# Kernel tuning notes

Hardware: AMD Instinct MI355X
Metric: run time of the kernel (lower is better)

Reference implementation:

```python
import jax, jax.numpy as jnp
import numpy as np
from jax.ops import segment_sum

N_NODES = 100000
N_EDGES = 1600000
N_LABEL = 200000
IN_C, HID_C, OUT_C = 128, 128, 64


def setup_inputs() -> dict:
    key = jax.random.key(0)
    ks = jax.random.split(key, 6)
    x = jax.random.normal(ks[0], (N_NODES, IN_C), dtype=jnp.float32)
    edge_index = jax.random.randint(ks[1], (2, N_EDGES), 0, N_NODES, dtype=jnp.int64)
    edge_label_index = jax.random.randint(ks[2], (2, N_LABEL), 0, N_NODES, dtype=jnp.int64)
    W1 = jax.random.normal(ks[3], (IN_C, HID_C), dtype=jnp.float32) / np.sqrt(IN_C)
    b1 = jnp.zeros((HID_C,), dtype=jnp.float32)
    W2 = jax.random.normal(ks[4], (HID_C, OUT_C), dtype=jnp.float32) / np.sqrt(HID_C)
    b2 = jnp.zeros((OUT_C,), dtype=jnp.float32)
    return {"x": x, "edge_index": edge_index, "edge_label_index": edge_label_index,
            "W1": W1, "b1": b1, "W2": W2, "b2": b2}


def gcn_conv(x, W, b, src, dst, num_nodes):
    # PyG GCNConv: linear transform, add self-loops, symmetric normalization, sum-aggregate, bias.
    h = x @ W                                            # [N, C_out]
    loop = jnp.arange(num_nodes, dtype=src.dtype)
    s = jnp.concatenate([src, loop])                     # [E + N]
    d = jnp.concatenate([dst, loop])
    deg = segment_sum(jnp.ones_like(d, dtype=h.dtype), d, num_segments=num_nodes)
    dinv = jnp.where(deg > 0, jax.lax.rsqrt(deg), 0.0)   # deg^-1/2
    norm = dinv[s] * dinv[d]                             # [E + N]
    msg = h[s] * norm[:, None]                           # gather + scale
    out = segment_sum(msg, d, num_segments=num_nodes)    # scatter-add aggregate
    return out + b


def reference(x, edge_index, edge_label_index, W1, b1, W2, b2):
    src, dst = edge_index[0], edge_index[1]
    n = x.shape[0]
    h = jax.nn.relu(gcn_conv(x, W1, b1, src, dst, n))
    z = gcn_conv(h, W2, b2, src, dst, n)                 # encode
    # decode: dot product over candidate edges
    return jnp.sum(z[edge_label_index[0]] * z[edge_label_index[1]], axis=-1)
```

## Files before the change

kernel.cpp:

```cpp
#include <hip/hip_runtime.h>

typedef __attribute__((ext_vector_type(8))) short bfrag8;
typedef __attribute__((ext_vector_type(4))) float facc4;

__device__ __forceinline__ unsigned int f2bf(float f) {
    unsigned int u = __float_as_uint(f);
    return (u + 0x7FFFu + ((u >> 16) & 1u)) >> 16;
}
__device__ __forceinline__ float bf_lo(unsigned int w) { return __uint_as_float(w << 16); }
__device__ __forceinline__ float bf_hi(unsigned int w) { return __uint_as_float(w & 0xffff0000u); }


__global__ void k_count(const int* __restrict__ dst, int* __restrict__ cnt,
                        unsigned int* __restrict__ pack, int e) {
    int i = blockIdx.x * blockDim.x + threadIdx.x;
    if (i < e) {
        int d = dst[i];
        int r = atomicAdd(&cnt[d], 1);
        pack[i] = ((unsigned int)d << 14) | (unsigned int)r;
    }
}


__global__ void k_cvt(const float* __restrict__ x, const float* __restrict__ W1,
                      const float* __restrict__ W2, unsigned short* __restrict__ x16,
                      unsigned short* __restrict__ w1t, unsigned short* __restrict__ w2t,
                      int nx8) {
    int t = blockIdx.x * blockDim.x + threadIdx.x;
    if (t < nx8) {
        const float4* xp = reinterpret_cast<const float4*>(x) + (long)t * 2;
        float4 a = xp[0], b = xp[1];
        uint4 o;
        o.x = f2bf(a.x) | (f2bf(a.y) << 16);
        o.y = f2bf(a.z) | (f2bf(a.w) << 16);
        o.z = f2bf(b.x) | (f2bf(b.y) << 16);
        o.w = f2bf(b.z) | (f2bf(b.w) << 16);
        reinterpret_cast<uint4*>(x16)[t] = o;
    } else {
        int u = t - nx8;
        if (u < 128 * 128) {
            int k = u >> 7, nn = u & 127;
            w1t[nn * 128 + k] = (unsigned short)f2bf(W1[u]);
        } else if ((u -= 128 * 128) < 128 * 64) {
            int k = u >> 6, nn = u & 63;
            w2t[nn * 128 + k] = (unsigned short)f2bf(W2[u]);
        }
    }
}

#define SCP 1024

__global__ void k_scan_a(const int* __restrict__ cnt, int* __restrict__ part, int n) {
    int p = blockIdx.x * blockDim.x + threadIdx.x;
    if (p >= SCP) return;
    int chunk = (n + SCP - 1) / SCP;
    int b = p * chunk, e = min(b + chunk, n), s = 0;
    for (int i = b; i < e; ++i) s += cnt[i];
    part[p] = s;
}

__global__ void k_scan_b(int* __restrict__ part) {
    __shared__ int sm[SCP];
    int t = threadIdx.x;
    sm[t] = part[t];
    __syncthreads();
    for (int off = 1; off < SCP; off <<= 1) {
        int v = (t >= off) ? sm[t - off] : 0;
        __syncthreads();
        sm[t] += v;
        __syncthreads();
    }
    part[t] = t ? sm[t - 1] : 0;
}

__global__ void k_scan_c(const int* __restrict__ cnt, const int* __restrict__ part,
                         int* __restrict__ rowptr, float* __restrict__ dinv, int n) {
    int p = blockIdx.x * blockDim.x + threadIdx.x;
    if (p >= SCP) return;
    int chunk = (n + SCP - 1) / SCP;
    int b = p * chunk, e = min(b + chunk, n);
    int run = part[p];
    for (int i = b; i < e; ++i) {
        rowptr[i] = run;
        dinv[i] = rsqrtf((float)(cnt[i] + 1));
        run += cnt[i];
    }
    if (p == SCP - 1) rowptr[n] = run;
}


#define FILL_G 192

__device__ __forceinline__ void fill_role(const int* __restrict__ src,
                                          const unsigned int* __restrict__ pack,
                                          const int* __restrict__ rowptr,
                                          int* __restrict__ csr_src,
                                          int e, float scale, int r, int g) {
    int chunk = (e + FILL_G - 1) / FILL_G;
    int beg = g * chunk, end = min(beg + chunk, e);
    for (int i = beg + threadIdx.x; i < end; i += blockDim.x) {
        unsigned int p = pack[i];
        int d = (int)(p >> 14);
        if ((int)((float)d * scale) == r) {
            int pos = rowptr[d] + (int)(p & 0x3FFFu);
            csr_src[pos] = src[i];
        }
    }
}


__global__ __launch_bounds__(256) void k_fuse(
        const int* __restrict__ src, const unsigned int* __restrict__ pack,
        const int* __restrict__ rowptr, int* __restrict__ csr_src, int e, float scale,
        const unsigned short* __restrict__ X16, const unsigned short* __restrict__ W1T,
        const float* __restrict__ dinv, unsigned short* __restrict__ H16, int n) {
    __shared__ unsigned short sA[128 * 64];
    __shared__ unsigned short sB[128 * 64];

    int t8 = blockIdx.x >> 3, l8 = blockIdx.x & 7;
    int m = t8 % 3, q = t8 / 3;

    if (m < 2) {
        int g = q * 2 + m;
        if (g < FILL_G)
            fill_role(src, pack, rowptr, csr_src, e, scale, l8, g);
        return;
    }

    int bid = q * 8 + l8;
    int row0 = bid * 128;
    if (row0 >= n) return;

    int tid = threadIdx.x;
    int lane = tid & 63;
    int wv = tid >> 6;

    facc4 acc[2][8];
#pragma unroll
    for (int i = 0; i < 2; ++i)
#pragma unroll
        for (int j = 0; j < 8; ++j) acc[i][j] = (facc4)0.f;

    for (int s = 0; s < 2; ++s) {
        if (s) __syncthreads();
#pragma unroll
        for (int it = 0; it < 4; ++it) {
            int chunk = it * 4 + wv;
            int L = chunk * 64 + lane;
            int row = L >> 3, gp = L & 7;
            int gsrc = gp ^ (row & 7);
            int grow = min(row0 + row, n - 1);
            const unsigned short* srcp = X16 + (long)grow * 128 + s * 64 + gsrc * 8;
            unsigned short* dstp = sA + chunk * 512;
            __builtin_amdgcn_global_load_lds(
                (const __attribute__((address_space(1))) void*)srcp,
                (__attribute__((address_space(3))) void*)dstp, 16, 0, 0);
        }
#pragma unroll
        for (int it = 0; it < 4; ++it) {
            int chunk = it * 4 + wv;
            int L = chunk * 64 + lane;
            int row = L >> 3, gp = L & 7;
            int gsrc = gp ^ (row & 7);
            const unsigned short* srcp = W1T + (long)row * 128 + s * 64 + gsrc * 8;
            unsigned short* dstp = sB + chunk * 512;
            __builtin_amdgcn_global_load_lds(
                (const __attribute__((address_space(1))) void*)srcp,
                (__attribute__((address_space(3))) void*)dstp, 16, 0, 0);
        }
        __syncthreads();

        bfrag8 af[2][2];
#pragma unroll
        for (int mt = 0; mt < 2; ++mt)
#pragma unroll
            for (int ks = 0; ks < 2; ++ks) {
                int r = wv * 32 + mt * 16 + (lane & 15);
                int g = ks * 4 + (lane >> 4);
                af[mt][ks] = *reinterpret_cast<const bfrag8*>(&sA[r * 64 + (g ^ (r & 7)) * 8]);
            }
#pragma unroll
        for (int nt = 0; nt < 8; ++nt) {
            int nr = nt * 16 + (lane & 15);
            bfrag8 b0 = *reinterpret_cast<const bfrag8*>(&sB[nr * 64 + (((lane >> 4)) ^ (nr & 7)) * 8]);
            bfrag8 b1 = *reinterpret_cast<const bfrag8*>(&sB[nr * 64 + ((4 + (lane >> 4)) ^ (nr & 7)) * 8]);
            acc[0][nt] = __builtin_amdgcn_mfma_f32_16x16x32_bf16(af[0][0], b0, acc[0][nt], 0, 0, 0);
            acc[1][nt] = __builtin_amdgcn_mfma_f32_16x16x32_bf16(af[1][0], b0, acc[1][nt], 0, 0, 0);
            acc[0][nt] = __builtin_amdgcn_mfma_f32_16x16x32_bf16(af[0][1], b1, acc[0][nt], 0, 0, 0);
            acc[1][nt] = __builtin_amdgcn_mfma_f32_16x16x32_bf16(af[1][1], b1, acc[1][nt], 0, 0, 0);
        }
    }

#pragma unroll
    for (int mt = 0; mt < 2; ++mt)
#pragma unroll
        for (int reg = 0; reg < 4; ++reg) {
            int r = row0 + wv * 32 + mt * 16 + (lane >> 4) * 4 + reg;
            if (r < n) {
                float dv = dinv[r];
#pragma unroll
                for (int nt = 0; nt < 8; ++nt)
                    H16[(long)r * 128 + nt * 16 + (lane & 15)] =
                        (unsigned short)f2bf(acc[mt][nt][reg] * dv);
            }
        }
}


__global__ __launch_bounds__(256) void k_gemmM64(const unsigned short* __restrict__ H16,
                                                 const unsigned short* __restrict__ W2T,
                                                 const float* __restrict__ dinv,
                                                 unsigned short* __restrict__ Z16, int n) {
    __shared__ unsigned short sA[128 * 64];
    __shared__ unsigned short sB[64 * 64];

    int row0 = blockIdx.x * 128;
    int tid = threadIdx.x;
    int lane = tid & 63;
    int wv = tid >> 6;

    facc4 acc[2][4];
#pragma unroll
    for (int i = 0; i < 2; ++i)
#pragma unroll
        for (int j = 0; j < 4; ++j) acc[i][j] = (facc4)0.f;

    for (int s = 0; s < 2; ++s) {
        if (s) __syncthreads();
#pragma unroll
        for (int it = 0; it < 4; ++it) {
            int chunk = it * 4 + wv;
            int L = chunk * 64 + lane;
            int row = L >> 3, gp = L & 7;
            int gsrc = gp ^ (row & 7);
            int grow = min(row0 + row, n - 1);
            const unsigned short* srcp = H16 + (long)grow * 128 + s * 64 + gsrc * 8;
            unsigned short* dstp = sA + chunk * 512;
            __builtin_amdgcn_global_load_lds(
                (const __attribute__((address_space(1))) void*)srcp,
                (__attribute__((address_space(3))) void*)dstp, 16, 0, 0);
        }
#pragma unroll
        for (int it = 0; it < 2; ++it) {
            int chunk = it * 4 + wv;
            int L = chunk * 64 + lane;
            int row = L >> 3, gp = L & 7;
            int gsrc = gp ^ (row & 7);
            const unsigned short* srcp = W2T + (long)row * 128 + s * 64 + gsrc * 8;
            unsigned short* dstp = sB + chunk * 512;
            __builtin_amdgcn_global_load_lds(
                (const __attribute__((address_space(1))) void*)srcp,
                (__attribute__((address_space(3))) void*)dstp, 16, 0, 0);
        }
        __syncthreads();

        bfrag8 af[2][2];
#pragma unroll
        for (int mt = 0; mt < 2; ++mt)
#pragma unroll
            for (int ks = 0; ks < 2; ++ks) {
                int r = wv * 32 + mt * 16 + (lane & 15);
                int g = ks * 4 + (lane >> 4);
                af[mt][ks] = *reinterpret_cast<const bfrag8*>(&sA[r * 64 + (g ^ (r & 7)) * 8]);
            }
#pragma unroll
        for (int nt = 0; nt < 4; ++nt) {
            int nr = nt * 16 + (lane & 15);
            bfrag8 b0 = *reinterpret_cast<const bfrag8*>(&sB[nr * 64 + (((lane >> 4)) ^ (nr & 7)) * 8]);
            bfrag8 b1 = *reinterpret_cast<const bfrag8*>(&sB[nr * 64 + ((4 + (lane >> 4)) ^ (nr & 7)) * 8]);
            acc[0][nt] = __builtin_amdgcn_mfma_f32_16x16x32_bf16(af[0][0], b0, acc[0][nt], 0, 0, 0);
            acc[1][nt] = __builtin_amdgcn_mfma_f32_16x16x32_bf16(af[1][0], b0, acc[1][nt], 0, 0, 0);
            acc[0][nt] = __builtin_amdgcn_mfma_f32_16x16x32_bf16(af[0][1], b1, acc[0][nt], 0, 0, 0);
            acc[1][nt] = __builtin_amdgcn_mfma_f32_16x16x32_bf16(af[1][1], b1, acc[1][nt], 0, 0, 0);
        }
    }

#pragma unroll
    for (int mt = 0; mt < 2; ++mt)
#pragma unroll
        for (int reg = 0; reg < 4; ++reg) {
            int r = row0 + wv * 32 + mt * 16 + (lane >> 4) * 4 + reg;
            if (r < n) {
                float dv = dinv[r];
#pragma unroll
                for (int nt = 0; nt < 4; ++nt)
                    Z16[(long)r * 64 + nt * 16 + (lane & 15)] =
                        (unsigned short)f2bf(acc[mt][nt][reg] * dv);
            }
        }
}


template<int C, bool RELU, bool OB>
__global__ void k_gather16(const int* __restrict__ rowptr, const int* __restrict__ csr_src,
                           const float* __restrict__ dinv, const unsigned short* __restrict__ h16,
                           const float* __restrict__ bias, void* __restrict__ outv, int n) {
    const int TPN = C / 8;
    const int RS = C / 8;
    int t = blockIdx.x * blockDim.x + threadIdx.x;
    int node = t / TPN;
    if (node >= n) return;
    int cg = t % TPN;

    const uint4* h4 = reinterpret_cast<const uint4*>(h16);
    float acc[8];
    {
        uint4 u = h4[(long)node * RS + cg];
        acc[0] = bf_lo(u.x); acc[1] = bf_hi(u.x);
        acc[2] = bf_lo(u.y); acc[3] = bf_hi(u.y);
        acc[4] = bf_lo(u.z); acc[5] = bf_hi(u.z);
        acc[6] = bf_lo(u.w); acc[7] = bf_hi(u.w);
    }

    int beg = rowptr[node], end = rowptr[node + 1];
    int e = beg;
    for (; e + 8 <= end; e += 8) {
        int s[8];
#pragma unroll
        for (int q = 0; q < 8; ++q) s[q] = csr_src[e + q];
        uint4 u[8];
#pragma unroll
        for (int q = 0; q < 8; ++q) u[q] = h4[(long)s[q] * RS + cg];
#pragma unroll
        for (int q = 0; q < 8; ++q) {
            acc[0] += bf_lo(u[q].x); acc[1] += bf_hi(u[q].x);
            acc[2] += bf_lo(u[q].y); acc[3] += bf_hi(u[q].y);
            acc[4] += bf_lo(u[q].z); acc[5] += bf_hi(u[q].z);
            acc[6] += bf_lo(u[q].w); acc[7] += bf_hi(u[q].w);
        }
    }
    for (; e < end; ++e) {
        uint4 u = h4[(long)csr_src[e] * RS + cg];
        acc[0] += bf_lo(u.x); acc[1] += bf_hi(u.x);
        acc[2] += bf_lo(u.y); acc[3] += bf_hi(u.y);
        acc[4] += bf_lo(u.z); acc[5] += bf_hi(u.z);
        acc[6] += bf_lo(u.w); acc[7] += bf_hi(u.w);
    }

    float dd = dinv[node];
    int c0 = cg * 8;
    float4 ba = *reinterpret_cast<const float4*>(bias + c0);
    float4 bb = *reinterpret_cast<const float4*>(bias + c0 + 4);
    float o[8];
    o[0] = fmaf(acc[0], dd, ba.x); o[1] = fmaf(acc[1], dd, ba.y);
    o[2] = fmaf(acc[2], dd, ba.z); o[3] = fmaf(acc[3], dd, ba.w);
    o[4] = fmaf(acc[4], dd, bb.x); o[5] = fmaf(acc[5], dd, bb.y);
    o[6] = fmaf(acc[6], dd, bb.z); o[7] = fmaf(acc[7], dd, bb.w);
    if (RELU) {
#pragma unroll
        for (int i = 0; i < 8; ++i) o[i] = fmaxf(o[i], 0.f);
    }
    if (OB) {
        uint4 w;
        w.x = f2bf(o[0]) | (f2bf(o[1]) << 16);
        w.y = f2bf(o[2]) | (f2bf(o[3]) << 16);
        w.z = f2bf(o[4]) | (f2bf(o[5]) << 16);
        w.w = f2bf(o[6]) | (f2bf(o[7]) << 16);
        *reinterpret_cast<uint4*>((unsigned short*)outv + (long)node * C + c0) = w;
    } else {
        float* of = (float*)outv + (long)node * C + c0;
        *reinterpret_cast<float4*>(of) = make_float4(o[0], o[1], o[2], o[3]);
        *reinterpret_cast<float4*>(of + 4) = make_float4(o[4], o[5], o[6], o[7]);
    }
}


__global__ void k_decode(const int* __restrict__ ia, const int* __restrict__ ib,
                         const float* __restrict__ z, float* __restrict__ out, int m) {
    int t = blockIdx.x * blockDim.x + threadIdx.x;
    int k = t / 16;
    if (k >= m) return;
    int c = (t & 15) * 4;
    int a = ia[k], b = ib[k];
    float4 va = *reinterpret_cast<const float4*>(z + (long)a * 64 + c);
    float4 vb = *reinterpret_cast<const float4*>(z + (long)b * 64 + c);
    float dot = va.x * vb.x + va.y * vb.y + va.z * vb.z + va.w * vb.w;
    dot += __shfl_xor(dot, 8);
    dot += __shfl_xor(dot, 4);
    dot += __shfl_xor(dot, 2);
    dot += __shfl_xor(dot, 1);
    if ((t & 15) == 0) out[k] = dot;
}


extern "C" void kernel_launch(void* const* d_in, const int* in_sizes, int n_in,
                              void* d_out, int out_size, void* d_ws, size_t ws_size,
                              hipStream_t stream) {
    const float* x  = (const float*)d_in[0];
    const int*   ei = (const int*)d_in[1];
    const int*   el = (const int*)d_in[2];
    const float* W1 = (const float*)d_in[3];
    const float* b1 = (const float*)d_in[4];
    const float* W2 = (const float*)d_in[5];
    const float* b2 = (const float*)d_in[6];
    float* out = (float*)d_out;

    const int N = in_sizes[0] / 128;
    const int E = in_sizes[1] / 2;
    const int L = out_size;

    const int* src = ei;
    const int* dst = ei + E;
    const int* la  = el;
    const int* lb  = el + L;

    char* wsb = (char*)d_ws;

    unsigned short* ht16 = (unsigned short*)wsb;
    unsigned short* zt16 = (unsigned short*)wsb;
    float*          zout = (float*)(wsb + (size_t)N * 128);

    unsigned int*   pack = (unsigned int*)(wsb + (size_t)N * 512);
    unsigned short* h16  = (unsigned short*)(wsb + (size_t)N * 512);
    unsigned short* x16  = (unsigned short*)(wsb + (size_t)N * 512 + (size_t)N * 256);

    int*   csr_src = (int*)(wsb + (size_t)N * 1024);
    int*   cnt     = csr_src + E;
    int*   rowptr  = cnt + N;
    float* dinv    = (float*)(rowptr + N + 1);
    int*   part    = (int*)(dinv + N);
    unsigned short* w1t = (unsigned short*)(part + SCP);
    unsigned short* w2t = w1t + 128 * 128;

    auto cdiv = [](long a, long b) { return (int)((a + b - 1) / b); };

    int nx8 = N * 16;
    k_cvt<<<cdiv((long)nx8 + 128 * 128 + 128 * 64, 256), 256, 0, stream>>>(
        x, W1, W2, x16, w1t, w2t, nx8);

    hipMemsetAsync(cnt, 0, (size_t)N * sizeof(int), stream);
    k_count <<<cdiv(E, 256), 256, 0, stream>>>(dst, cnt, pack, E);
    k_scan_a<<<SCP / 256, 256, 0, stream>>>(cnt, part, N);
    k_scan_b<<<1, SCP, 0, stream>>>(part);
    k_scan_c<<<SCP / 256, 256, 0, stream>>>(cnt, part, rowptr, dinv, N);

    k_fuse<<<294 * 8, 256, 0, stream>>>(src, pack, rowptr, csr_src, E, 8.0f / (float)N,
                                        x16, w1t, dinv, ht16, N);

    k_gather16<128, true, true><<<cdiv((long)N * 16, 256), 256, 0, stream>>>(
        rowptr, csr_src, dinv, ht16, b1, h16, N);

    k_gemmM64<<<cdiv(N, 128), 256, 0, stream>>>(h16, w2t, dinv, zt16, N);
    k_gather16<64, false, false><<<cdiv((long)N * 8, 256), 256, 0, stream>>>(
        rowptr, csr_src, dinv, zt16, b2, zout, N);

    k_decode<<<cdiv((long)L * 16, 256), 256, 0, stream>>>(la, lb, zout, out, L);
}
```

Measured before the change: 328.5 us.

## Fuse degree count into prep kernel, use atomic cursors, store z in bf16

The separate count kernel is folded into the conversion kernel as extra blocks. Those blocks bucket destination nodes into eight range partitions for atomic locality, and no longer write a packed rank array. The CSR fill now gets slots through atomic cursors initialised by the scan instead of precomputed ranks. The second-layer output is stored as bf16, and decode reads bf16 rows, which halves gather traffic at the cost of precision. Atomic-based fill makes the order within each CSR row nondeterministic and adds atomics in the fill pass.

```diff
diff --git a/kernel.cpp b/kernel.cpp
--- a/kernel.cpp
+++ b/kernel.cpp
@@ -11,30 +11,33 @@
 __device__ __forceinline__ float bf_hi(unsigned int w) { return __uint_as_float(w & 0xffff0000u); }
 
 
-__global__ void k_count(const int* __restrict__ dst, int* __restrict__ cnt,
-                        unsigned int* __restrict__ pack, int e) {
-    int i = blockIdx.x * blockDim.x + threadIdx.x;
-    if (i < e) {
-        int d = dst[i];
-        int r = atomicAdd(&cnt[d], 1);
-        pack[i] = ((unsigned int)d << 14) | (unsigned int)r;
-    }
-}
-
-
-__global__ void k_cvt(const float* __restrict__ x, const float* __restrict__ W1,
-                      const float* __restrict__ W2, unsigned short* __restrict__ x16,
-                      unsigned short* __restrict__ w1t, unsigned short* __restrict__ w2t,
-                      int nx8) {
-    int t = blockIdx.x * blockDim.x + threadIdx.x;
+#define CNT_G 192
+
+__global__ void k_prep(const float* __restrict__ x, const float* __restrict__ W1,
+                       const float* __restrict__ W2, unsigned short* __restrict__ x16,
+                       unsigned short* __restrict__ w1t, unsigned short* __restrict__ w2t,
+                       const int* __restrict__ dst, int* __restrict__ cnt,
+                       int e, int nx8, float scale) {
+    int b = blockIdx.x;
+    if (b < 8 * CNT_G) {
+        int r = b & 7, g = b >> 3;
+        int chunk = (e + CNT_G - 1) / CNT_G;
+        int beg = g * chunk, end = min(beg + chunk, e);
+        for (int i = beg + threadIdx.x; i < end; i += blockDim.x) {
+            int d = dst[i];
+            if ((int)((float)d * scale) == r) atomicAdd(&cnt[d], 1);
+        }
+        return;
+    }
+    int t = (b - 8 * CNT_G) * blockDim.x + threadIdx.x;
     if (t < nx8) {
         const float4* xp = reinterpret_cast<const float4*>(x) + (long)t * 2;
-        float4 a = xp[0], b = xp[1];
+        float4 a = xp[0], v = xp[1];
         uint4 o;
         o.x = f2bf(a.x) | (f2bf(a.y) << 16);
         o.y = f2bf(a.z) | (f2bf(a.w) << 16);
-        o.z = f2bf(b.x) | (f2bf(b.y) << 16);
-        o.w = f2bf(b.z) | (f2bf(b.w) << 16);
+        o.z = f2bf(v.x) | (f2bf(v.y) << 16);
+        o.w = f2bf(v.z) | (f2bf(v.w) << 16);
         reinterpret_cast<uint4*>(x16)[t] = o;
     } else {
         int u = t - nx8;
@@ -74,7 +77,8 @@
 }
 
 __global__ void k_scan_c(const int* __restrict__ cnt, const int* __restrict__ part,
-                         int* __restrict__ rowptr, float* __restrict__ dinv, int n) {
+                         int* __restrict__ rowptr, int* __restrict__ cursor,
+                         float* __restrict__ dinv, int n) {
     int p = blockIdx.x * blockDim.x + threadIdx.x;
     if (p >= SCP) return;
     int chunk = (n + SCP - 1) / SCP;
@@ -82,6 +86,7 @@
     int run = part[p];
     for (int i = b; i < e; ++i) {
         rowptr[i] = run;
+        cursor[i] = run;
         dinv[i] = rsqrtf((float)(cnt[i] + 1));
         run += cnt[i];
     }
@@ -92,17 +97,16 @@
 #define FILL_G 192
 
 __device__ __forceinline__ void fill_role(const int* __restrict__ src,
-                                          const unsigned int* __restrict__ pack,
-                                          const int* __restrict__ rowptr,
+                                          const int* __restrict__ dstv,
+                                          int* __restrict__ cursor,
                                           int* __restrict__ csr_src,
                                           int e, float scale, int r, int g) {
     int chunk = (e + FILL_G - 1) / FILL_G;
     int beg = g * chunk, end = min(beg + chunk, e);
     for (int i = beg + threadIdx.x; i < end; i += blockDim.x) {
-        unsigned int p = pack[i];
-        int d = (int)(p >> 14);
+        int d = dstv[i];
         if ((int)((float)d * scale) == r) {
-            int pos = rowptr[d] + (int)(p & 0x3FFFu);
+            int pos = atomicAdd(&cursor[d], 1);
             csr_src[pos] = src[i];
         }
     }
@@ -110,8 +114,8 @@
 
 
 __global__ __launch_bounds__(256) void k_fuse(
-        const int* __restrict__ src, const unsigned int* __restrict__ pack,
-        const int* __restrict__ rowptr, int* __restrict__ csr_src, int e, float scale,
+        const int* __restrict__ src, const int* __restrict__ dstv,
+        int* __restrict__ cursor, int* __restrict__ csr_src, int e, float scale,
         const unsigned short* __restrict__ X16, const unsigned short* __restrict__ W1T,
         const float* __restrict__ dinv, unsigned short* __restrict__ H16, int n) {
     __shared__ unsigned short sA[128 * 64];
@@ -123,7 +127,7 @@
     if (m < 2) {
         int g = q * 2 + m;
         if (g < FILL_G)
-            fill_role(src, pack, rowptr, csr_src, e, scale, l8, g);
+            fill_role(src, dstv, cursor, csr_src, e, scale, l8, g);
         return;
     }
 
@@ -365,21 +369,24 @@
 }
 
 
-__global__ void k_decode(const int* __restrict__ ia, const int* __restrict__ ib,
-                         const float* __restrict__ z, float* __restrict__ out, int m) {
+__global__ void k_decode16(const int* __restrict__ ia, const int* __restrict__ ib,
+                           const unsigned short* __restrict__ z, float* __restrict__ out, int m) {
     int t = blockIdx.x * blockDim.x + threadIdx.x;
-    int k = t / 16;
+    int k = t >> 3;
     if (k >= m) return;
-    int c = (t & 15) * 4;
+    int cg = t & 7;
     int a = ia[k], b = ib[k];
-    float4 va = *reinterpret_cast<const float4*>(z + (long)a * 64 + c);
-    float4 vb = *reinterpret_cast<const float4*>(z + (long)b * 64 + c);
-    float dot = va.x * vb.x + va.y * vb.y + va.z * vb.z + va.w * vb.w;
-    dot += __shfl_xor(dot, 8);
+    const uint4* z4 = reinterpret_cast<const uint4*>(z);
+    uint4 ua = z4[(long)a * 8 + cg];
+    uint4 ub = z4[(long)b * 8 + cg];
+    float dot = bf_lo(ua.x) * bf_lo(ub.x) + bf_hi(ua.x) * bf_hi(ub.x)
+              + bf_lo(ua.y) * bf_lo(ub.y) + bf_hi(ua.y) * bf_hi(ub.y)
+              + bf_lo(ua.z) * bf_lo(ub.z) + bf_hi(ua.z) * bf_hi(ub.z)
+              + bf_lo(ua.w) * bf_lo(ub.w) + bf_hi(ua.w) * bf_hi(ub.w);
     dot += __shfl_xor(dot, 4);
     dot += __shfl_xor(dot, 2);
     dot += __shfl_xor(dot, 1);
-    if ((t & 15) == 0) out[k] = dot;
+    if (cg == 0) out[k] = dot;
 }
 
 
@@ -408,41 +415,41 @@
 
     unsigned short* ht16 = (unsigned short*)wsb;
     unsigned short* zt16 = (unsigned short*)wsb;
-    float*          zout = (float*)(wsb + (size_t)N * 128);
-
-    unsigned int*   pack = (unsigned int*)(wsb + (size_t)N * 512);
+    unsigned short* z16  = (unsigned short*)(wsb + (size_t)N * 256);
+
     unsigned short* h16  = (unsigned short*)(wsb + (size_t)N * 512);
     unsigned short* x16  = (unsigned short*)(wsb + (size_t)N * 512 + (size_t)N * 256);
 
     int*   csr_src = (int*)(wsb + (size_t)N * 1024);
     int*   cnt     = csr_src + E;
     int*   rowptr  = cnt + N;
-    float* dinv    = (float*)(rowptr + N + 1);
+    int*   cursor  = rowptr + N + 1;
+    float* dinv    = (float*)(cursor + N);
     int*   part    = (int*)(dinv + N);
     unsigned short* w1t = (unsigned short*)(part + SCP);
     unsigned short* w2t = w1t + 128 * 128;
 
     auto cdiv = [](long a, long b) { return (int)((a + b - 1) / b); };
 
+    hipMemsetAsync(cnt, 0, (size_t)N * sizeof(int), stream);
     int nx8 = N * 16;
-    k_cvt<<<cdiv((long)nx8 + 128 * 128 + 128 * 64, 256), 256, 0, stream>>>(
-        x, W1, W2, x16, w1t, w2t, nx8);
-
-    hipMemsetAsync(cnt, 0, (size_t)N * sizeof(int), stream);
-    k_count <<<cdiv(E, 256), 256, 0, stream>>>(dst, cnt, pack, E);
+    int cvtB = cdiv((long)nx8 + 128 * 128 + 128 * 64, 256);
+    k_prep<<<8 * CNT_G + cvtB, 256, 0, stream>>>(x, W1, W2, x16, w1t, w2t,
+                                                 dst, cnt, E, nx8, 8.0f / (float)N);
+
     k_scan_a<<<SCP / 256, 256, 0, stream>>>(cnt, part, N);
     k_scan_b<<<1, SCP, 0, stream>>>(part);
-    k_scan_c<<<SCP / 256, 256, 0, stream>>>(cnt, part, rowptr, dinv, N);
-
-    k_fuse<<<294 * 8, 256, 0, stream>>>(src, pack, rowptr, csr_src, E, 8.0f / (float)N,
+    k_scan_c<<<SCP / 256, 256, 0, stream>>>(cnt, part, rowptr, cursor, dinv, N);
+
+    k_fuse<<<294 * 8, 256, 0, stream>>>(src, dst, cursor, csr_src, E, 8.0f / (float)N,
                                         x16, w1t, dinv, ht16, N);
 
     k_gather16<128, true, true><<<cdiv((long)N * 16, 256), 256, 0, stream>>>(
         rowptr, csr_src, dinv, ht16, b1, h16, N);
 
     k_gemmM64<<<cdiv(N, 128), 256, 0, stream>>>(h16, w2t, dinv, zt16, N);
-    k_gather16<64, false, false><<<cdiv((long)N * 8, 256), 256, 0, stream>>>(
-        rowptr, csr_src, dinv, zt16, b2, zout, N);
-
-    k_decode<<<cdiv((long)L * 16, 256), 256, 0, stream>>>(la, lb, zout, out, L);
-}
+    k_gather16<64, false, true><<<cdiv((long)N * 8, 256), 256, 0, stream>>>(
+        rowptr, csr_src, dinv, zt16, b2, z16, N);
+
+    k_decode16<<<cdiv((long)L * 8, 256), 256, 0, stream>>>(la, lb, z16, out, L);
+}
```

New measurement: 352.2 us. 1.07x slower.
